# Optimization experiments

Hardware: AMD Instinct MI355X
Metric: run time of the kernel (lower is better)

Reference implementation:

```python
import jax, jax.numpy as jnp
import numpy as np

H = 16
N_JOBS = 1000000
N_MACH = 500000
NEG = -1e8

PARAM_SHAPES = [("jW1",(H,H)),("jb1",(H,)),("jW2",(H,H)),("jb2",(H,)),
                ("mW1",(H,H)),("mb1",(H,)),("mW2",(H,H)),("mb2",(H,)),
                ("aj_Wq",(H,H)),("aj_bq",(H,)),("aj_Wr",(H,H)),("aj_V",(H,)),
                ("am_Wq",(H,H)),("am_bq",(H,)),("am_Wr",(H,H)),("am_V",(H,)),
                ("ja_Wq",(H,H)),("ja_bq",(H,)),("ja_Wr",(H,H)),("ja_V",(H,)),
                ("ma_Wq",(H,H)),("ma_bq",(H,)),("ma_Wr",(H,H)),("ma_V",(H,)),
                ("g1W",(H,3*H)),("g1b",(H,)),("g2W",(H,3*H)),("g2b",(H,)),
                ("last_j",(H,))]

def setup_inputs() -> dict:
    key = jax.random.key(0)
    inp = {}
    inp["jobs"] = jax.random.normal(jax.random.fold_in(key, 0), (N_JOBS, H), dtype=jnp.float32)
    inp["machines"] = jax.random.normal(jax.random.fold_in(key, 1), (N_MACH, H), dtype=jnp.float32)
    inp["alloc_jobs_mask"] = jax.random.randint(jax.random.fold_in(key, 2), (N_JOBS,), 0, 2) > 0
    for i, (name, shape) in enumerate(PARAM_SHAPES):
        inp[name] = jax.random.normal(jax.random.fold_in(key, 10 + i), shape, dtype=jnp.float32) * 0.05
    return inp

def _emb(x, W1, b1, W2, b2):
    # custom_embedding: two tanh MLP layers (torch Linear: x @ W.T + b)
    h = jnp.tanh(x @ W1.T + b1)
    return jnp.tanh(h @ W2.T + b2)

def _att_logits(q, ref, Wq, bq, Wr, V):
    # Bahdanau additive attention: tanh(W_q q + W_r ref) @ V -> [S]
    return jnp.tanh((q @ Wq.T + bq) + ref @ Wr.T) @ V

def _query_att(q, ref, Wq, bq, Wr, V):
    # Attention with use_softmax=True followed by weighted sum over ref
    w = jax.nn.softmax(_att_logits(q, ref, Wq, bq, Wr, V))
    return w @ ref  # [H]

def reference(jobs, machines, alloc_jobs_mask,
              jW1, jb1, jW2, jb2, mW1, mb1, mW2, mb2,
              aj_Wq, aj_bq, aj_Wr, aj_V, am_Wq, am_bq, am_Wr, am_V,
              ja_Wq, ja_bq, ja_Wr, ja_V, ma_Wq, ma_bq, ma_Wr, ma_V,
              g1W, g1b, g2W, g2b, last_j):
    E_j = _emb(jobs, jW1, jb1, jW2, jb2)        # [Sj, H]
    E_m = _emb(machines, mW1, mb1, mW2, mb2)    # [Sm, H]

    # glimpse 1 conditioned on last_j
    g_j1 = _query_att(last_j, E_j, aj_Wq, aj_bq, aj_Wr, aj_V)
    g_m1 = _query_att(last_j, E_m, am_Wq, am_bq, am_Wr, am_V)
    g1 = jnp.tanh(jnp.concatenate([last_j, g_j1, g_m1]) @ g1W.T + g1b)

    # job pointer logits + invalid-action masking
    j_logits = _att_logits(g1, E_j, ja_Wq, ja_bq, ja_Wr, ja_V)
    j_logits = jnp.where(alloc_jobs_mask, j_logits, NEG)
    sel_j = jnp.argmax(j_logits)
    e_js = E_j[sel_j]

    # glimpse 2 conditioned on selected job embedding
    g_j2 = _query_att(e_js, E_j, aj_Wq, aj_bq, aj_Wr, aj_V)
    g_m2 = _query_att(e_js, E_m, am_Wq, am_bq, am_Wr, am_V)
    g2 = jnp.tanh(jnp.concatenate([e_js, g_j2, g_m2]) @ g2W.T + g2b)

    m_logits = _att_logits(g2, E_m, ma_Wq, ma_bq, ma_Wr, ma_V)
    sel_m = jnp.argmax(m_logits)

    logpas = jax.nn.log_softmax(j_logits)[sel_j] + jax.nn.log_softmax(m_logits)[sel_m]
    return sel_j, sel_m, logpas
```

## Files before the change

### kernel.cpp

```cpp
#include <hip/hip_runtime.h>
#include <cstddef>
#include <cstdint>


constexpr int NJ = 1000000;
constexpr int NM = 500000;
constexpr float NEGV = -1e8f;

constexpr int BLK = 256;
constexpr int ROWS_PER_BLK = 512;
constexpr int GB_J2 = (NJ + ROWS_PER_BLK - 1) / ROWS_PER_BLK;
constexpr int GB_M2 = (NM + ROWS_PER_BLK - 1) / ROWS_PER_BLK;
constexpr int GB_TOT2 = GB_J2 + GB_M2;

constexpr int S_QKJA = 0;
constexpr int S_QK2J = 16;
constexpr int S_QK2M = 32;
constexpr int S_EJS  = 48;
constexpr int S_QKMA = 64;
constexpr int S_LOGPJ = 80;
constexpr int S_SELJ  = 81;
constexpr int P1J = 128;
constexpr int P1M = P1J + GB_J2 * 17;
constexpr int P2V = P1M + GB_M2 * 17;
constexpr int P2I = P2V + GB_J2;
constexpr int P2L = P2I + GB_J2;

typedef float v2f __attribute__((ext_vector_type(2)));

struct Params {
    const float *jobs, *machines;
    const int *mask;
    const float *jW1, *jb1, *jW2, *jb2;
    const float *mW1, *mb1, *mW2, *mb2;
    const float *aj_Wq, *aj_bq, *aj_Wr, *aj_V;
    const float *am_Wq, *am_bq, *am_Wr, *am_V;
    const float *ja_Wq, *ja_bq, *ja_Wr, *ja_V;
    const float *ma_Wq, *ma_bq, *ma_Wr, *ma_V;
    const float *g1W, *g1b, *g2W, *g2b, *last_j;
    float *S;
    float *out;
};


__device__ __forceinline__ float fast_tanh(float x) {
    float e = __builtin_amdgcn_exp2f(x * 2.8853900817779268f);
    float r = __builtin_amdgcn_rcpf(e + 1.0f);
    return fmaf(-2.0f, r, 1.0f);
}

__device__ __forceinline__ v2f vbc(float a) { v2f r; r.x = a; r.y = a; return r; }

__device__ __forceinline__ v2f vfma(float w, v2f b, v2f c) {
    return __builtin_elementwise_fma(vbc(w), b, c);
}
__device__ __forceinline__ v2f vfma2(v2f a, v2f b, v2f c) {
    return __builtin_elementwise_fma(a, b, c);
}
__device__ __forceinline__ v2f vtanh(v2f a) {
    v2f r; r.x = fast_tanh(a.x); r.y = fast_tanh(a.y); return r;
}

__device__ __forceinline__ void load16(const float* __restrict__ X, size_t r, float (&x)[16]) {
    const float4* p4 = reinterpret_cast<const float4*>(X) + r * 4;
    float4 a = p4[0], b = p4[1], c = p4[2], d = p4[3];
    x[0]=a.x; x[1]=a.y; x[2]=a.z; x[3]=a.w;
    x[4]=b.x; x[5]=b.y; x[6]=b.z; x[7]=b.w;
    x[8]=c.x; x[9]=c.y; x[10]=c.z; x[11]=c.w;
    x[12]=d.x; x[13]=d.y; x[14]=d.z; x[15]=d.w;
}

__device__ __forceinline__ void load16_v2(const float* __restrict__ X, size_t rA, size_t rB,
                                          v2f (&x)[16]) {
    float a[16], b[16];
    load16(X, rA, a);
    load16(X, rB, b);
#pragma unroll
    for (int k = 0; k < 16; ++k) { x[k].x = a[k]; x[k].y = b[k]; }
}

__device__ __forceinline__ void emb16_v2(const v2f (&x)[16],
                                         const float* __restrict__ W1, const float* __restrict__ b1,
                                         const float* __restrict__ W2, const float* __restrict__ b2,
                                         v2f (&e)[16]) {
    v2f h[16];
#pragma unroll
    for (int i = 0; i < 16; ++i) {
        v2f a = vbc(b1[i]);
#pragma unroll
        for (int k = 0; k < 16; ++k) a = vfma(W1[i * 16 + k], x[k], a);
        h[i] = vtanh(a);
    }
#pragma unroll
    for (int i = 0; i < 16; ++i) {
        v2f a = vbc(b2[i]);
#pragma unroll
        for (int k = 0; k < 16; ++k) a = vfma(W2[i * 16 + k], h[k], a);
        e[i] = vtanh(a);
    }
}

__device__ __forceinline__ v2f att_logit_v2(const v2f (&e)[16], const float (&qk)[16],
                                            const float* __restrict__ Wr,
                                            const float* __restrict__ V) {
    v2f acc = vbc(0.0f);
#pragma unroll
    for (int i = 0; i < 16; ++i) {
        v2f r = vbc(qk[i]);
#pragma unroll
        for (int k = 0; k < 16; ++k) r = vfma(Wr[i * 16 + k], e[k], r);
        acc = vfma2(vbc(V[i]), vtanh(r), acc);
    }
    return acc;
}

__device__ __forceinline__ float wave_reduce_sum(float v) {
#pragma unroll
    for (int off = 32; off > 0; off >>= 1) v += __shfl_xor(v, off, 64);
    return v;
}

__device__ __forceinline__ void wave_reduce_argmax(float &v, int &idx) {
#pragma unroll
    for (int off = 32; off > 0; off >>= 1) {
        float ov = __shfl_xor(v, off, 64);
        int oi = __shfl_xor(idx, off, 64);
        if (ov > v || (ov == v && oi < idx)) { v = ov; idx = oi; }
    }
}

__device__ __forceinline__ float block_sum(float v) {
    __shared__ float sm[4];
    v = wave_reduce_sum(v);
    __syncthreads();
    if ((threadIdx.x & 63) == 0) sm[threadIdx.x >> 6] = v;
    __syncthreads();
    return sm[0] + sm[1] + sm[2] + sm[3];
}

__device__ __forceinline__ void block_argmax(float &v, int &i) {
    __shared__ float sv[4];
    __shared__ int si[4];
    wave_reduce_argmax(v, i);
    __syncthreads();
    if ((threadIdx.x & 63) == 0) { sv[threadIdx.x >> 6] = v; si[threadIdx.x >> 6] = i; }
    __syncthreads();
    float bv = sv[0]; int bi = si[0];
#pragma unroll
    for (int k = 1; k < 4; ++k)
        if (sv[k] > bv || (sv[k] == bv && si[k] < bi)) { bv = sv[k]; bi = si[k]; }
    v = bv; i = bi;
}

__device__ __forceinline__ void block_sum17(float l, const float (&s)[16], float* dst) {
    const int lane = threadIdx.x & 63;
    float c[8];
#pragma unroll
    for (int j = 0; j < 8; ++j) {
        const bool hi = lane & 1;
        float t = __shfl_xor(hi ? s[j] : s[j + 8], 1, 64);
        c[j] = (hi ? s[j + 8] : s[j]) + t;
    }
    float d[4];
#pragma unroll
    for (int j = 0; j < 4; ++j) {
        const bool hi = lane & 2;
        float t = __shfl_xor(hi ? c[j] : c[j + 4], 2, 64);
        d[j] = (hi ? c[j + 4] : c[j]) + t;
    }
    float e2[2];
#pragma unroll
    for (int j = 0; j < 2; ++j) {
        const bool hi = lane & 4;
        float t = __shfl_xor(hi ? d[j] : d[j + 2], 4, 64);
        e2[j] = (hi ? d[j + 2] : d[j]) + t;
    }
    float f;
    {
        const bool hi = lane & 8;
        float t = __shfl_xor(hi ? e2[0] : e2[1], 8, 64);
        f = (hi ? e2[1] : e2[0]) + t;
    }
    f += __shfl_xor(f, 16, 64);
    f += __shfl_xor(f, 32, 64);
#pragma unroll
    for (int off = 32; off > 0; off >>= 1) l += __shfl_xor(l, off, 64);

    const int idx = ((lane & 1) << 3) | ((lane & 2) << 1) | ((lane & 4) >> 1) | ((lane & 8) >> 3);
    __shared__ float red[4][17];
    const int w = threadIdx.x >> 6;
    __syncthreads();
    if (lane < 16) red[w][1 + idx] = f;
    if (lane == 0) red[w][0] = l;
    __syncthreads();
    if (threadIdx.x < 17)
        dst[threadIdx.x] = red[0][threadIdx.x] + red[1][threadIdx.x] + red[2][threadIdx.x] + red[3][threadIdx.x];
}

__global__ __launch_bounds__(BLK) void k_sweepA(Params p) {
    const bool isJob = blockIdx.x < GB_J2;
    const float* X  = isJob ? p.jobs : p.machines;
    const float* W1 = isJob ? p.jW1 : p.mW1;
    const float* b1 = isJob ? p.jb1 : p.mb1;
    const float* W2 = isJob ? p.jW2 : p.mW2;
    const float* b2 = isJob ? p.jb2 : p.mb2;
    const float* Wr = isJob ? p.aj_Wr : p.am_Wr;
    const float* V  = isJob ? p.aj_V  : p.am_V;
    const int n  = isJob ? NJ : NM;
    const int b0 = isJob ? (int)blockIdx.x : (int)blockIdx.x - GB_J2;

    __shared__ float qks[16];
    if (threadIdx.x < 16) {
        const float* Wq = isJob ? p.aj_Wq : p.am_Wq;
        const float* bq = isJob ? p.aj_bq : p.am_bq;
        const int i = threadIdx.x;
        float a = bq[i];
#pragma unroll
        for (int k = 0; k < 16; ++k) a = fmaf(Wq[i * 16 + k], p.last_j[k], a);
        qks[i] = a;
    }
    __syncthreads();
    float qk[16];
#pragma unroll
    for (int i = 0; i < 16; ++i) qk[i] = qks[i];

    const int r0 = b0 * ROWS_PER_BLK + 2 * (int)threadIdx.x;
    const bool v = r0 < n;
    const size_t a0 = (size_t)(v ? r0 : 0);
    const size_t a1 = a0 + (v ? 1 : 0);

    v2f x[16], e[16];
    load16_v2(X, a0, a1, x);
    emb16_v2(x, W1, b1, W2, b2, e);
    v2f lg = att_logit_v2(e, qk, Wr, V);
    float pw0 = v ? __expf(lg.x) : 0.0f;
    float pw1 = v ? __expf(lg.y) : 0.0f;
    float l = pw0 + pw1, s[16];
#pragma unroll
    for (int i = 0; i < 16; ++i) s[i] = fmaf(pw0, e[i].x, pw1 * e[i].y);

    block_sum17(l, s, p.S + (isJob ? P1J : P1M) + (size_t)b0 * 17);
}

__global__ __launch_bounds__(BLK) void k_combine_g(Params p, int phase) {
    const float* PJ = p.S + P1J;
    const float* PM = p.S + P1M;
    float lJ = 0.0f, lM = 0.0f, sJ[16], sM[16];
#pragma unroll
    for (int c = 0; c < 16; ++c) { sJ[c] = 0.0f; sM[c] = 0.0f; }
    for (int i = threadIdx.x; i < GB_J2; i += BLK) {
        lJ += PJ[i * 17];
#pragma unroll
        for (int c = 0; c < 16; ++c) sJ[c] += PJ[i * 17 + 1 + c];
    }
    for (int i = threadIdx.x; i < GB_M2; i += BLK) {
        lM += PM[i * 17];
#pragma unroll
        for (int c = 0; c < 16; ++c) sM[c] += PM[i * 17 + 1 + c];
    }
    __shared__ float totJ[17], totM[17];
    block_sum17(lJ, sJ, totJ);
    block_sum17(lM, sM, totM);
    __syncthreads();

    __shared__ float cb[48], gbuf[16];
    if (threadIdx.x < 16) {
        int i = threadIdx.x;
        cb[i]      = phase ? p.S[S_EJS + i] : p.last_j[i];
        cb[16 + i] = totJ[1 + i] / totJ[0];
        cb[32 + i] = totM[1 + i] / totM[0];
    }
    __syncthreads();
    const float* gW  = phase ? p.g2W : p.g1W;
    const float* gbv = phase ? p.g2b : p.g1b;
    if (threadIdx.x < 16) {
        int i = threadIdx.x;
        float a = gbv[i];
#pragma unroll
        for (int k = 0; k < 48; ++k) a = fmaf(gW[i * 48 + k], cb[k], a);
        gbuf[i] = fast_tanh(a);
    }
    __syncthreads();
    const float* Wq = phase ? p.ma_Wq : p.ja_Wq;
    const float* bq = phase ? p.ma_bq : p.ja_bq;
    const int off = phase ? S_QKMA : S_QKJA;
    if (threadIdx.x < 16) {
        int i = threadIdx.x;
        float a = bq[i];
#pragma unroll
        for (int k = 0; k < 16; ++k) a = fmaf(Wq[i * 16 + k], gbuf[k], a);
        p.S[off + i] = a;
    }
}

__global__ __launch_bounds__(BLK) void k_sweepB(Params p) {
    float qk[16];
#pragma unroll
    for (int i = 0; i < 16; ++i) qk[i] = p.S[S_QKJA + i];

    const int r0 = blockIdx.x * ROWS_PER_BLK + 2 * (int)threadIdx.x;
    const bool v = r0 < NJ;
    const size_t a0 = (size_t)(v ? r0 : 0);
    const size_t a1 = a0 + (v ? 1 : 0);

    v2f x[16], e[16];
    load16_v2(p.jobs, a0, a1, x);
    emb16_v2(x, p.jW1, p.jb1, p.jW2, p.jb2, e);
    v2f lg = att_logit_v2(e, qk, p.ja_Wr, p.ja_V);

    int2 mq = make_int2(0, 0);
    if (v) mq = *reinterpret_cast<const int2*>(p.mask + r0);
    const bool m0 = v && (mq.x != 0);
    const bool m1 = v && (mq.y != 0);
    float l = (m0 ? __expf(lg.x) : 0.0f) + (m1 ? __expf(lg.y) : 0.0f);
    float am0 = m0 ? lg.x : NEGV - 1.0f;
    float am1 = m1 ? lg.y : NEGV - 1.0f;
    float best;
    int bi;
    if (am0 >= am1) { best = am0; bi = r0; }
    else            { best = am1; bi = r0 + 1; }

    l = wave_reduce_sum(l);
    wave_reduce_argmax(best, bi);
    __shared__ float rl[4], rv[4];
    __shared__ int ri[4];
    int w = threadIdx.x >> 6, ln = threadIdx.x & 63;
    if (ln == 0) { rl[w] = l; rv[w] = best; ri[w] = bi; }
    __syncthreads();
    if (threadIdx.x == 0) {
        float L = rl[0] + rl[1] + rl[2] + rl[3];
        float vv = rv[0]; int i = ri[0];
#pragma unroll
        for (int k = 1; k < 4; ++k)
            if (rv[k] > vv || (rv[k] == vv && ri[k] < i)) { vv = rv[k]; i = ri[k]; }
        p.S[P2V + blockIdx.x] = vv;
        p.S[P2I + blockIdx.x] = (float)i;
        p.S[P2L + blockIdx.x] = L;
    }
}

__global__ __launch_bounds__(BLK) void k_combine2(Params p) {
    float v = -3.4e38f; int vi = 0x7fffffff; float l = 0.0f;
    for (int i = threadIdx.x; i < GB_J2; i += BLK) {
        float pv = p.S[P2V + i];
        int pi = (int)p.S[P2I + i];
        if (pv > v || (pv == v && pi < vi)) { v = pv; vi = pi; }
        l += p.S[P2L + i];
    }
    l = block_sum(l);
    block_argmax(v, vi);
    const int sel = vi;

    __shared__ float xb[16], hb[16], eb[16];
    if (threadIdx.x < 16) xb[threadIdx.x] = p.jobs[(size_t)sel * 16 + threadIdx.x];
    __syncthreads();
    if (threadIdx.x < 16) {
        int i = threadIdx.x;
        float a = p.jb1[i];
#pragma unroll
        for (int k = 0; k < 16; ++k) a = fmaf(p.jW1[i * 16 + k], xb[k], a);
        hb[i] = fast_tanh(a);
    }
    __syncthreads();
    if (threadIdx.x < 16) {
        int i = threadIdx.x;
        float a = p.jb2[i];
#pragma unroll
        for (int k = 0; k < 16; ++k) a = fmaf(p.jW2[i * 16 + k], hb[k], a);
        float e = fast_tanh(a);
        eb[i] = e;
        p.S[S_EJS + i] = e;
    }
    __syncthreads();
    if (threadIdx.x < 16) {
        int i = threadIdx.x;
        float a1 = p.aj_bq[i], a2 = p.am_bq[i];
#pragma unroll
        for (int k = 0; k < 16; ++k) {
            a1 = fmaf(p.aj_Wq[i * 16 + k], eb[k], a1);
            a2 = fmaf(p.am_Wq[i * 16 + k], eb[k], a2);
        }
        p.S[S_QK2J + i] = a1;
        p.S[S_QK2M + i] = a2;
    }
    if (threadIdx.x == 0) {
        p.S[S_LOGPJ] = v - logf(l);
        p.S[S_SELJ] = (float)sel;
    }
}

__global__ __launch_bounds__(BLK) void k_sweepC(Params p) {
    const bool isJob = blockIdx.x < GB_J2;
    const float* X  = isJob ? p.jobs : p.machines;
    const float* W1 = isJob ? p.jW1 : p.mW1;
    const float* b1 = isJob ? p.jb1 : p.mb1;
    const float* W2 = isJob ? p.jW2 : p.mW2;
    const float* b2 = isJob ? p.jb2 : p.mb2;
    const float* Wr = isJob ? p.aj_Wr : p.am_Wr;
    const float* V  = isJob ? p.aj_V  : p.am_V;
    const int n  = isJob ? NJ : NM;
    const int b0 = isJob ? (int)blockIdx.x : (int)blockIdx.x - GB_J2;
    const int qoff = isJob ? S_QK2J : S_QK2M;

    float qk[16];
#pragma unroll
    for (int i = 0; i < 16; ++i) qk[i] = p.S[qoff + i];

    const int r0 = b0 * ROWS_PER_BLK + 2 * (int)threadIdx.x;
    const bool v = r0 < n;
    const size_t a0 = (size_t)(v ? r0 : 0);
    const size_t a1 = a0 + (v ? 1 : 0);

    v2f x[16], e[16];
    load16_v2(X, a0, a1, x);
    emb16_v2(x, W1, b1, W2, b2, e);
    v2f lg = att_logit_v2(e, qk, Wr, V);
    float pw0 = v ? __expf(lg.x) : 0.0f;
    float pw1 = v ? __expf(lg.y) : 0.0f;
    float l = pw0 + pw1, s[16];
#pragma unroll
    for (int i = 0; i < 16; ++i) s[i] = fmaf(pw0, e[i].x, pw1 * e[i].y);

    block_sum17(l, s, p.S + (isJob ? P1J : P1M) + (size_t)b0 * 17);
}

__global__ __launch_bounds__(BLK) void k_sweepD(Params p) {
    float qk[16];
#pragma unroll
    for (int i = 0; i < 16; ++i) qk[i] = p.S[S_QKMA + i];

    const int r0 = blockIdx.x * ROWS_PER_BLK + 2 * (int)threadIdx.x;
    const bool v = r0 < NM;
    const size_t a0 = (size_t)(v ? r0 : 0);
    const size_t a1 = a0 + (v ? 1 : 0);

    v2f x[16], e[16];
    load16_v2(p.machines, a0, a1, x);
    emb16_v2(x, p.mW1, p.mb1, p.mW2, p.mb2, e);
    v2f lg = att_logit_v2(e, qk, p.ma_Wr, p.ma_V);
    float l = (v ? __expf(lg.x) : 0.0f) + (v ? __expf(lg.y) : 0.0f);
    float am0 = v ? lg.x : -3.4e38f;
    float am1 = v ? lg.y : -3.4e38f;
    float best;
    int bi;
    if (am0 >= am1) { best = am0; bi = r0; }
    else            { best = am1; bi = r0 + 1; }

    l = wave_reduce_sum(l);
    wave_reduce_argmax(best, bi);
    __shared__ float rl[4], rv[4];
    __shared__ int ri[4];
    int w = threadIdx.x >> 6, ln = threadIdx.x & 63;
    if (ln == 0) { rl[w] = l; rv[w] = best; ri[w] = bi; }
    __syncthreads();
    if (threadIdx.x == 0) {
        float L = rl[0] + rl[1] + rl[2] + rl[3];
        float vv = rv[0]; int i = ri[0];
#pragma unroll
        for (int k = 1; k < 4; ++k)
            if (rv[k] > vv || (rv[k] == vv && ri[k] < i)) { vv = rv[k]; i = ri[k]; }
        p.S[P2V + blockIdx.x] = vv;
        p.S[P2I + blockIdx.x] = (float)i;
        p.S[P2L + blockIdx.x] = L;
    }
}

__global__ __launch_bounds__(BLK) void k_combine4(Params p) {
    float v = -3.4e38f; int vi = 0x7fffffff; float l = 0.0f;
    for (int i = threadIdx.x; i < GB_M2; i += BLK) {
        float pv = p.S[P2V + i];
        int pi = (int)p.S[P2I + i];
        if (pv > v || (pv == v && pi < vi)) { v = pv; vi = pi; }
        l += p.S[P2L + i];
    }
    l = block_sum(l);
    block_argmax(v, vi);
    if (threadIdx.x == 0) {
        p.out[0] = p.S[S_SELJ];
        p.out[1] = (float)vi;
        p.out[2] = p.S[S_LOGPJ] + (v - logf(l));
    }
}

extern "C" void kernel_launch(void* const* d_in, const int* in_sizes, int n_in,
                              void* d_out, int out_size, void* d_ws, size_t ws_size,
                              hipStream_t stream) {
    Params p;
    p.jobs     = (const float*)d_in[0];
    p.machines = (const float*)d_in[1];
    p.mask     = (const int*)d_in[2];
    p.jW1 = (const float*)d_in[3];  p.jb1 = (const float*)d_in[4];
    p.jW2 = (const float*)d_in[5];  p.jb2 = (const float*)d_in[6];
    p.mW1 = (const float*)d_in[7];  p.mb1 = (const float*)d_in[8];
    p.mW2 = (const float*)d_in[9];  p.mb2 = (const float*)d_in[10];
    p.aj_Wq = (const float*)d_in[11]; p.aj_bq = (const float*)d_in[12];
    p.aj_Wr = (const float*)d_in[13]; p.aj_V  = (const float*)d_in[14];
    p.am_Wq = (const float*)d_in[15]; p.am_bq = (const float*)d_in[16];
    p.am_Wr = (const float*)d_in[17]; p.am_V  = (const float*)d_in[18];
    p.ja_Wq = (const float*)d_in[19]; p.ja_bq = (const float*)d_in[20];
    p.ja_Wr = (const float*)d_in[21]; p.ja_V  = (const float*)d_in[22];
    p.ma_Wq = (const float*)d_in[23]; p.ma_bq = (const float*)d_in[24];
    p.ma_Wr = (const float*)d_in[25]; p.ma_V  = (const float*)d_in[26];
    p.g1W = (const float*)d_in[27]; p.g1b = (const float*)d_in[28];
    p.g2W = (const float*)d_in[29]; p.g2b = (const float*)d_in[30];
    p.last_j = (const float*)d_in[31];
    p.S = (float*)d_ws;
    p.out = (float*)d_out;

    k_sweepA<<<GB_TOT2, BLK, 0, stream>>>(p);
    k_combine_g<<<1, BLK, 0, stream>>>(p, 0);
    k_sweepB<<<GB_J2, BLK, 0, stream>>>(p);
    k_combine2<<<1, BLK, 0, stream>>>(p);
    k_sweepC<<<GB_TOT2, BLK, 0, stream>>>(p);
    k_combine_g<<<1, BLK, 0, stream>>>(p, 1);
    k_sweepD<<<GB_M2, BLK, 0, stream>>>(p);
    k_combine4<<<1, BLK, 0, stream>>>(p);
}
```

Baseline: 336.0 us.

## Cache embeddings in workspace and fold combine kernels into last-block reductions

The first sweep now writes the computed job and machine embeddings to a workspace cache in a coalesced per-block layout, so the later sweeps read 16 floats per row instead of recomputing the two-layer tanh MLP. The cache is used only when the workspace is large enough. Each single-block combine kernel is replaced by a last-block-done pattern (atomic counter plus threadfence), which removes four kernel launches. A small zero kernel resets the counters and precomputes the first query projections. The trade-off is extra memory traffic for writing and re-reading about 96 MB of embeddings, plus a serial tail in the last block of each sweep.

```diff
diff --git a/kernel.cpp b/kernel.cpp
--- a/kernel.cpp
+++ b/kernel.cpp
@@ -12,6 +12,7 @@
 constexpr int GB_J2 = (NJ + ROWS_PER_BLK - 1) / ROWS_PER_BLK;
 constexpr int GB_M2 = (NM + ROWS_PER_BLK - 1) / ROWS_PER_BLK;
 constexpr int GB_TOT2 = GB_J2 + GB_M2;
+constexpr int EBLK = ROWS_PER_BLK * 16;
 
 constexpr int S_QKJA = 0;
 constexpr int S_QK2J = 16;
@@ -20,11 +21,16 @@
 constexpr int S_QKMA = 64;
 constexpr int S_LOGPJ = 80;
 constexpr int S_SELJ  = 81;
+constexpr int C_CTR   = 84;
+constexpr int S_QK1J  = 96;
+constexpr int S_QK1M  = 112;
 constexpr int P1J = 128;
 constexpr int P1M = P1J + GB_J2 * 17;
 constexpr int P2V = P1M + GB_M2 * 17;
 constexpr int P2I = P2V + GB_J2;
 constexpr int P2L = P2I + GB_J2;
+constexpr size_t E_OFF = 65536;
+static_assert(P2L + GB_J2 <= (int)E_OFF, "partials overflow into E cache");
 
 typedef float v2f __attribute__((ext_vector_type(2)));
 
@@ -39,6 +45,7 @@
     const float *ma_Wq, *ma_bq, *ma_Wr, *ma_V;
     const float *g1W, *g1b, *g2W, *g2b, *last_j;
     float *S;
+    float *Ej, *Em;
     float *out;
 };
 
@@ -79,6 +86,22 @@
     for (int k = 0; k < 16; ++k) { x[k].x = a[k]; x[k].y = b[k]; }
 }
 
+__device__ __forceinline__ void ecache_store(float* __restrict__ Eb, int t, const v2f (&e)[16]) {
+    float4* p4 = reinterpret_cast<float4*>(Eb);
+#pragma unroll
+    for (int kp = 0; kp < 8; ++kp)
+        p4[kp * 256 + t] = make_float4(e[2*kp].x, e[2*kp].y, e[2*kp+1].x, e[2*kp+1].y);
+}
+__device__ __forceinline__ void ecache_load(const float* __restrict__ Eb, int t, v2f (&e)[16]) {
+    const float4* p4 = reinterpret_cast<const float4*>(Eb);
+#pragma unroll
+    for (int kp = 0; kp < 8; ++kp) {
+        float4 q = p4[kp * 256 + t];
+        e[2*kp].x = q.x;   e[2*kp].y = q.y;
+        e[2*kp+1].x = q.z; e[2*kp+1].y = q.w;
+    }
+}
+
 __device__ __forceinline__ void emb16_v2(const v2f (&x)[16],
                                          const float* __restrict__ W1, const float* __restrict__ b1,
                                          const float* __restrict__ W2, const float* __restrict__ b2,
@@ -197,6 +220,151 @@
         dst[threadIdx.x] = red[0][threadIdx.x] + red[1][threadIdx.x] + red[2][threadIdx.x] + red[3][threadIdx.x];
 }
 
+__device__ __forceinline__ bool last_block(int* ctr, int nblocks) {
+    __shared__ int lastFlag;
+    __syncthreads();
+    __threadfence();
+    if (threadIdx.x == 0) lastFlag = (atomicAdd(ctr, 1) == nblocks - 1);
+    __syncthreads();
+    if (!lastFlag) return false;
+    __threadfence();
+    return true;
+}
+
+
+__device__ __forceinline__ void combine_g_body(const Params& p, int phase) {
+    const float* PJ = p.S + P1J;
+    const float* PM = p.S + P1M;
+    float lJ = 0.0f, lM = 0.0f, sJ[16], sM[16];
+#pragma unroll
+    for (int c = 0; c < 16; ++c) { sJ[c] = 0.0f; sM[c] = 0.0f; }
+    for (int i = threadIdx.x; i < GB_J2; i += BLK) {
+        lJ += PJ[i * 17];
+#pragma unroll
+        for (int c = 0; c < 16; ++c) sJ[c] += PJ[i * 17 + 1 + c];
+    }
+    for (int i = threadIdx.x; i < GB_M2; i += BLK) {
+        lM += PM[i * 17];
+#pragma unroll
+        for (int c = 0; c < 16; ++c) sM[c] += PM[i * 17 + 1 + c];
+    }
+    __shared__ float totJ[17], totM[17];
+    block_sum17(lJ, sJ, totJ);
+    block_sum17(lM, sM, totM);
+    __syncthreads();
+
+    __shared__ float cb[48], gbuf[16];
+    if (threadIdx.x < 16) {
+        int i = threadIdx.x;
+        cb[i]      = phase ? p.S[S_EJS + i] : p.last_j[i];
+        cb[16 + i] = totJ[1 + i] / totJ[0];
+        cb[32 + i] = totM[1 + i] / totM[0];
+    }
+    __syncthreads();
+    const float* gW  = phase ? p.g2W : p.g1W;
+    const float* gbv = phase ? p.g2b : p.g1b;
+    if (threadIdx.x < 16) {
+        int i = threadIdx.x;
+        float a = gbv[i];
+#pragma unroll
+        for (int k = 0; k < 48; ++k) a = fmaf(gW[i * 48 + k], cb[k], a);
+        gbuf[i] = fast_tanh(a);
+    }
+    __syncthreads();
+    const float* Wq = phase ? p.ma_Wq : p.ja_Wq;
+    const float* bq = phase ? p.ma_bq : p.ja_bq;
+    const int off = phase ? S_QKMA : S_QKJA;
+    if (threadIdx.x < 16) {
+        int i = threadIdx.x;
+        float a = bq[i];
+#pragma unroll
+        for (int k = 0; k < 16; ++k) a = fmaf(Wq[i * 16 + k], gbuf[k], a);
+        p.S[off + i] = a;
+    }
+}
+
+__device__ __forceinline__ void combine2_body(const Params& p) {
+    float v = -3.4e38f; int vi = 0x7fffffff; float l = 0.0f;
+    for (int i = threadIdx.x; i < GB_J2; i += BLK) {
+        float pv = p.S[P2V + i];
+        int pi = (int)p.S[P2I + i];
+        if (pv > v || (pv == v && pi < vi)) { v = pv; vi = pi; }
+        l += p.S[P2L + i];
+    }
+    l = block_sum(l);
+    block_argmax(v, vi);
+    const int sel = vi;
+
+    __shared__ float xb[16], hb[16], eb[16];
+    if (threadIdx.x < 16) xb[threadIdx.x] = p.jobs[(size_t)sel * 16 + threadIdx.x];
+    __syncthreads();
+    if (threadIdx.x < 16) {
+        int i = threadIdx.x;
+        float a = p.jb1[i];
+#pragma unroll
+        for (int k = 0; k < 16; ++k) a = fmaf(p.jW1[i * 16 + k], xb[k], a);
+        hb[i] = fast_tanh(a);
+    }
+    __syncthreads();
+    if (threadIdx.x < 16) {
+        int i = threadIdx.x;
+        float a = p.jb2[i];
+#pragma unroll
+        for (int k = 0; k < 16; ++k) a = fmaf(p.jW2[i * 16 + k], hb[k], a);
+        float e = fast_tanh(a);
+        eb[i] = e;
+        p.S[S_EJS + i] = e;
+    }
+    __syncthreads();
+    if (threadIdx.x < 16) {
+        int i = threadIdx.x;
+        float a1 = p.aj_bq[i], a2 = p.am_bq[i];
+#pragma unroll
+        for (int k = 0; k < 16; ++k) {
+            a1 = fmaf(p.aj_Wq[i * 16 + k], eb[k], a1);
+            a2 = fmaf(p.am_Wq[i * 16 + k], eb[k], a2);
+        }
+        p.S[S_QK2J + i] = a1;
+        p.S[S_QK2M + i] = a2;
+    }
+    if (threadIdx.x == 0) {
+        p.S[S_LOGPJ] = v - logf(l);
+        p.S[S_SELJ] = (float)sel;
+    }
+}
+
+__device__ __forceinline__ void combine4_body(const Params& p) {
+    float v = -3.4e38f; int vi = 0x7fffffff; float l = 0.0f;
+    for (int i = threadIdx.x; i < GB_M2; i += BLK) {
+        float pv = p.S[P2V + i];
+        int pi = (int)p.S[P2I + i];
+        if (pv > v || (pv == v && pi < vi)) { v = pv; vi = pi; }
+        l += p.S[P2L + i];
+    }
+    l = block_sum(l);
+    block_argmax(v, vi);
+    if (threadIdx.x == 0) {
+        p.out[0] = p.S[S_SELJ];
+        p.out[1] = (float)vi;
+        p.out[2] = p.S[S_LOGPJ] + (v - logf(l));
+    }
+}
+
+__global__ __launch_bounds__(64) void k_zero(Params p) {
+    if (threadIdx.x < 32) {
+        const bool isJ = threadIdx.x < 16;
+        const int i = threadIdx.x & 15;
+        const float* Wq = isJ ? p.aj_Wq : p.am_Wq;
+        const float* bq = isJ ? p.aj_bq : p.am_bq;
+        float a = bq[i];
+#pragma unroll
+        for (int k = 0; k < 16; ++k) a = fmaf(Wq[i * 16 + k], p.last_j[k], a);
+        p.S[(isJ ? S_QK1J : S_QK1M) + i] = a;
+    }
+    if (threadIdx.x >= 60) reinterpret_cast<int*>(p.S + C_CTR)[threadIdx.x - 60] = 0;
+}
+
+template <bool CACHE>
 __global__ __launch_bounds__(BLK) void k_sweepA(Params p) {
     const bool isJob = blockIdx.x < GB_J2;
     const float* X  = isJob ? p.jobs : p.machines;
@@ -206,23 +374,16 @@
     const float* b2 = isJob ? p.jb2 : p.mb2;
     const float* Wr = isJob ? p.aj_Wr : p.am_Wr;
     const float* V  = isJob ? p.aj_V  : p.am_V;
+    float* E = isJob ? p.Ej : p.Em;
     const int n  = isJob ? NJ : NM;
     const int b0 = isJob ? (int)blockIdx.x : (int)blockIdx.x - GB_J2;
 
-    __shared__ float qks[16];
-    if (threadIdx.x < 16) {
-        const float* Wq = isJob ? p.aj_Wq : p.am_Wq;
-        const float* bq = isJob ? p.aj_bq : p.am_bq;
-        const int i = threadIdx.x;
-        float a = bq[i];
-#pragma unroll
-        for (int k = 0; k < 16; ++k) a = fmaf(Wq[i * 16 + k], p.last_j[k], a);
-        qks[i] = a;
-    }
-    __syncthreads();
     float qk[16];
-#pragma unroll
-    for (int i = 0; i < 16; ++i) qk[i] = qks[i];
+    {
+        const float* src = p.S + (isJob ? S_QK1J : S_QK1M);
+#pragma unroll
+        for (int i = 0; i < 16; ++i) qk[i] = src[i];
+    }
 
     const int r0 = b0 * ROWS_PER_BLK + 2 * (int)threadIdx.x;
     const bool v = r0 < n;
@@ -232,6 +393,7 @@
     v2f x[16], e[16];
     load16_v2(X, a0, a1, x);
     emb16_v2(x, W1, b1, W2, b2, e);
+    if (CACHE) ecache_store(E + (size_t)b0 * EBLK, (int)threadIdx.x, e);
     v2f lg = att_logit_v2(e, qk, Wr, V);
     float pw0 = v ? __expf(lg.x) : 0.0f;
     float pw1 = v ? __expf(lg.y) : 0.0f;
@@ -240,59 +402,12 @@
     for (int i = 0; i < 16; ++i) s[i] = fmaf(pw0, e[i].x, pw1 * e[i].y);
 
     block_sum17(l, s, p.S + (isJob ? P1J : P1M) + (size_t)b0 * 17);
-}
-
-__global__ __launch_bounds__(BLK) void k_combine_g(Params p, int phase) {
-    const float* PJ = p.S + P1J;
-    const float* PM = p.S + P1M;
-    float lJ = 0.0f, lM = 0.0f, sJ[16], sM[16];
-#pragma unroll
-    for (int c = 0; c < 16; ++c) { sJ[c] = 0.0f; sM[c] = 0.0f; }
-    for (int i = threadIdx.x; i < GB_J2; i += BLK) {
-        lJ += PJ[i * 17];
-#pragma unroll
-        for (int c = 0; c < 16; ++c) sJ[c] += PJ[i * 17 + 1 + c];
-    }
-    for (int i = threadIdx.x; i < GB_M2; i += BLK) {
-        lM += PM[i * 17];
-#pragma unroll
-        for (int c = 0; c < 16; ++c) sM[c] += PM[i * 17 + 1 + c];
-    }
-    __shared__ float totJ[17], totM[17];
-    block_sum17(lJ, sJ, totJ);
-    block_sum17(lM, sM, totM);
-    __syncthreads();
-
-    __shared__ float cb[48], gbuf[16];
-    if (threadIdx.x < 16) {
-        int i = threadIdx.x;
-        cb[i]      = phase ? p.S[S_EJS + i] : p.last_j[i];
-        cb[16 + i] = totJ[1 + i] / totJ[0];
-        cb[32 + i] = totM[1 + i] / totM[0];
-    }
-    __syncthreads();
-    const float* gW  = phase ? p.g2W : p.g1W;
-    const float* gbv = phase ? p.g2b : p.g1b;
-    if (threadIdx.x < 16) {
-        int i = threadIdx.x;
-        float a = gbv[i];
-#pragma unroll
-        for (int k = 0; k < 48; ++k) a = fmaf(gW[i * 48 + k], cb[k], a);
-        gbuf[i] = fast_tanh(a);
-    }
-    __syncthreads();
-    const float* Wq = phase ? p.ma_Wq : p.ja_Wq;
-    const float* bq = phase ? p.ma_bq : p.ja_bq;
-    const int off = phase ? S_QKMA : S_QKJA;
-    if (threadIdx.x < 16) {
-        int i = threadIdx.x;
-        float a = bq[i];
-#pragma unroll
-        for (int k = 0; k < 16; ++k) a = fmaf(Wq[i * 16 + k], gbuf[k], a);
-        p.S[off + i] = a;
-    }
-}
-
+
+    if (last_block(reinterpret_cast<int*>(p.S + C_CTR) + 0, GB_TOT2))
+        combine_g_body(p, 0);
+}
+
+template <bool CACHE>
 __global__ __launch_bounds__(BLK) void k_sweepB(Params p) {
     float qk[16];
 #pragma unroll
@@ -303,9 +418,14 @@
     const size_t a0 = (size_t)(v ? r0 : 0);
     const size_t a1 = a0 + (v ? 1 : 0);
 
-    v2f x[16], e[16];
-    load16_v2(p.jobs, a0, a1, x);
-    emb16_v2(x, p.jW1, p.jb1, p.jW2, p.jb2, e);
+    v2f e[16];
+    if (CACHE) {
+        ecache_load(p.Ej + (size_t)blockIdx.x * EBLK, (int)threadIdx.x, e);
+    } else {
+        v2f x[16];
+        load16_v2(p.jobs, a0, a1, x);
+        emb16_v2(x, p.jW1, p.jb1, p.jW2, p.jb2, e);
+    }
     v2f lg = att_logit_v2(e, qk, p.ja_Wr, p.ja_V);
 
     int2 mq = make_int2(0, 0);
@@ -337,67 +457,22 @@
         p.S[P2I + blockIdx.x] = (float)i;
         p.S[P2L + blockIdx.x] = L;
     }
-}
-
-__global__ __launch_bounds__(BLK) void k_combine2(Params p) {
-    float v = -3.4e38f; int vi = 0x7fffffff; float l = 0.0f;
-    for (int i = threadIdx.x; i < GB_J2; i += BLK) {
-        float pv = p.S[P2V + i];
-        int pi = (int)p.S[P2I + i];
-        if (pv > v || (pv == v && pi < vi)) { v = pv; vi = pi; }
-        l += p.S[P2L + i];
-    }
-    l = block_sum(l);
-    block_argmax(v, vi);
-    const int sel = vi;
-
-    __shared__ float xb[16], hb[16], eb[16];
-    if (threadIdx.x < 16) xb[threadIdx.x] = p.jobs[(size_t)sel * 16 + threadIdx.x];
-    __syncthreads();
-    if (threadIdx.x < 16) {
-        int i = threadIdx.x;
-        float a = p.jb1[i];
-#pragma unroll
-        for (int k = 0; k < 16; ++k) a = fmaf(p.jW1[i * 16 + k], xb[k], a);
-        hb[i] = fast_tanh(a);
-    }
-    __syncthreads();
-    if (threadIdx.x < 16) {
-        int i = threadIdx.x;
-        float a = p.jb2[i];
-#pragma unroll
-        for (int k = 0; k < 16; ++k) a = fmaf(p.jW2[i * 16 + k], hb[k], a);
-        float e = fast_tanh(a);
-        eb[i] = e;
-        p.S[S_EJS + i] = e;
-    }
-    __syncthreads();
-    if (threadIdx.x < 16) {
-        int i = threadIdx.x;
-        float a1 = p.aj_bq[i], a2 = p.am_bq[i];
-#pragma unroll
-        for (int k = 0; k < 16; ++k) {
-            a1 = fmaf(p.aj_Wq[i * 16 + k], eb[k], a1);
-            a2 = fmaf(p.am_Wq[i * 16 + k], eb[k], a2);
-        }
-        p.S[S_QK2J + i] = a1;
-        p.S[S_QK2M + i] = a2;
-    }
-    if (threadIdx.x == 0) {
-        p.S[S_LOGPJ] = v - logf(l);
-        p.S[S_SELJ] = (float)sel;
-    }
-}
-
+
+    if (last_block(reinterpret_cast<int*>(p.S + C_CTR) + 1, GB_J2))
+        combine2_body(p);
+}
+
+template <bool CACHE>
 __global__ __launch_bounds__(BLK) void k_sweepC(Params p) {
     const bool isJob = blockIdx.x < GB_J2;
+    const float* Wr = isJob ? p.aj_Wr : p.am_Wr;
+    const float* V  = isJob ? p.aj_V  : p.am_V;
+    const float* E  = isJob ? p.Ej : p.Em;
     const float* X  = isJob ? p.jobs : p.machines;
     const float* W1 = isJob ? p.jW1 : p.mW1;
     const float* b1 = isJob ? p.jb1 : p.mb1;
     const float* W2 = isJob ? p.jW2 : p.mW2;
     const float* b2 = isJob ? p.jb2 : p.mb2;
-    const float* Wr = isJob ? p.aj_Wr : p.am_Wr;
-    const float* V  = isJob ? p.aj_V  : p.am_V;
     const int n  = isJob ? NJ : NM;
     const int b0 = isJob ? (int)blockIdx.x : (int)blockIdx.x - GB_J2;
     const int qoff = isJob ? S_QK2J : S_QK2M;
@@ -411,9 +486,14 @@
     const size_t a0 = (size_t)(v ? r0 : 0);
     const size_t a1 = a0 + (v ? 1 : 0);
 
-    v2f x[16], e[16];
-    load16_v2(X, a0, a1, x);
-    emb16_v2(x, W1, b1, W2, b2, e);
+    v2f e[16];
+    if (CACHE) {
+        ecache_load(E + (size_t)b0 * EBLK, (int)threadIdx.x, e);
+    } else {
+        v2f x[16];
+        load16_v2(X, a0, a1, x);
+        emb16_v2(x, W1, b1, W2, b2, e);
+    }
     v2f lg = att_logit_v2(e, qk, Wr, V);
     float pw0 = v ? __expf(lg.x) : 0.0f;
     float pw1 = v ? __expf(lg.y) : 0.0f;
@@ -422,8 +502,12 @@
     for (int i = 0; i < 16; ++i) s[i] = fmaf(pw0, e[i].x, pw1 * e[i].y);
 
     block_sum17(l, s, p.S + (isJob ? P1J : P1M) + (size_t)b0 * 17);
-}
-
+
+    if (last_block(reinterpret_cast<int*>(p.S + C_CTR) + 2, GB_TOT2))
+        combine_g_body(p, 1);
+}
+
+template <bool CACHE>
 __global__ __launch_bounds__(BLK) void k_sweepD(Params p) {
     float qk[16];
 #pragma unroll
@@ -434,9 +518,14 @@
     const size_t a0 = (size_t)(v ? r0 : 0);
     const size_t a1 = a0 + (v ? 1 : 0);
 
-    v2f x[16], e[16];
-    load16_v2(p.machines, a0, a1, x);
-    emb16_v2(x, p.mW1, p.mb1, p.mW2, p.mb2, e);
+    v2f e[16];
+    if (CACHE) {
+        ecache_load(p.Em + (size_t)blockIdx.x * EBLK, (int)threadIdx.x, e);
+    } else {
+        v2f x[16];
+        load16_v2(p.machines, a0, a1, x);
+        emb16_v2(x, p.mW1, p.mb1, p.mW2, p.mb2, e);
+    }
     v2f lg = att_logit_v2(e, qk, p.ma_Wr, p.ma_V);
     float l = (v ? __expf(lg.x) : 0.0f) + (v ? __expf(lg.y) : 0.0f);
     float am0 = v ? lg.x : -3.4e38f;
@@ -463,23 +552,9 @@
         p.S[P2I + blockIdx.x] = (float)i;
         p.S[P2L + blockIdx.x] = L;
     }
-}
-
-__global__ __launch_bounds__(BLK) void k_combine4(Params p) {
-    float v = -3.4e38f; int vi = 0x7fffffff; float l = 0.0f;
-    for (int i = threadIdx.x; i < GB_M2; i += BLK) {
-        float pv = p.S[P2V + i];
-        int pi = (int)p.S[P2I + i];
-        if (pv > v || (pv == v && pi < vi)) { v = pv; vi = pi; }
-        l += p.S[P2L + i];
-    }
-    l = block_sum(l);
-    block_argmax(v, vi);
-    if (threadIdx.x == 0) {
-        p.out[0] = p.S[S_SELJ];
-        p.out[1] = (float)vi;
-        p.out[2] = p.S[S_LOGPJ] + (v - logf(l));
-    }
+
+    if (last_block(reinterpret_cast<int*>(p.S + C_CTR) + 3, GB_M2))
+        combine4_body(p);
 }
 
 extern "C" void kernel_launch(void* const* d_in, const int* in_sizes, int n_in,
@@ -505,14 +580,23 @@
     p.g2W = (const float*)d_in[29]; p.g2b = (const float*)d_in[30];
     p.last_j = (const float*)d_in[31];
     p.S = (float*)d_ws;
+    p.Ej = (float*)d_ws + E_OFF;
+    p.Em = p.Ej + (size_t)GB_J2 * EBLK;
     p.out = (float*)d_out;
 
-    k_sweepA<<<GB_TOT2, BLK, 0, stream>>>(p);
-    k_combine_g<<<1, BLK, 0, stream>>>(p, 0);
-    k_sweepB<<<GB_J2, BLK, 0, stream>>>(p);
-    k_combine2<<<1, BLK, 0, stream>>>(p);
-    k_sweepC<<<GB_TOT2, BLK, 0, stream>>>(p);
-    k_combine_g<<<1, BLK, 0, stream>>>(p, 1);
-    k_sweepD<<<GB_M2, BLK, 0, stream>>>(p);
-    k_combine4<<<1, BLK, 0, stream>>>(p);
-}
+    const size_t needed = (E_OFF + (size_t)GB_TOT2 * EBLK) * sizeof(float);
+    const bool cache = ws_size >= needed;
+
+    k_zero<<<1, 64, 0, stream>>>(p);
+    if (cache) {
+        k_sweepA<true><<<GB_TOT2, BLK, 0, stream>>>(p);
+        k_sweepB<true><<<GB_J2, BLK, 0, stream>>>(p);
+        k_sweepC<true><<<GB_TOT2, BLK, 0, stream>>>(p);
+        k_sweepD<true><<<GB_M2, BLK, 0, stream>>>(p);
+    } else {
+        k_sweepA<false><<<GB_TOT2, BLK, 0, stream>>>(p);
+        k_sweepB<false><<<GB_J2, BLK, 0, stream>>>(p);
+        k_sweepC<false><<<GB_TOT2, BLK, 0, stream>>>(p);
+        k_sweepD<false><<<GB_M2, BLK, 0, stream>>>(p);
+    }
+}
```

New measurement: 1.022 ms. 204% more time.

## Cache job and machine embeddings in workspace and reuse them across sweeps

Applied to the files above, without the earlier changes.

The first sweep now writes the computed job and machine embeddings to a workspace buffer in a coalesced float4 layout. The three later sweeps load those embeddings instead of re-reading the raw inputs and re-running the two-layer tanh MLP. This removes repeated embedding arithmetic, which dominates these sweeps. The cost is an extra write of all embeddings in the first pass and a dependence on a large workspace; without enough space the code falls back to recomputing.

```diff
diff --git a/kernel.cpp b/kernel.cpp
--- a/kernel.cpp
+++ b/kernel.cpp
@@ -12,6 +12,7 @@
 constexpr int GB_J2 = (NJ + ROWS_PER_BLK - 1) / ROWS_PER_BLK;
 constexpr int GB_M2 = (NM + ROWS_PER_BLK - 1) / ROWS_PER_BLK;
 constexpr int GB_TOT2 = GB_J2 + GB_M2;
+constexpr int EBLK = ROWS_PER_BLK * 16;
 
 constexpr int S_QKJA = 0;
 constexpr int S_QK2J = 16;
@@ -25,6 +26,8 @@
 constexpr int P2V = P1M + GB_M2 * 17;
 constexpr int P2I = P2V + GB_J2;
 constexpr int P2L = P2I + GB_J2;
+constexpr size_t E_OFF = 65536;
+static_assert(P2L + GB_J2 <= (int)E_OFF, "partials overflow into E cache");
 
 typedef float v2f __attribute__((ext_vector_type(2)));
 
@@ -39,6 +42,7 @@
     const float *ma_Wq, *ma_bq, *ma_Wr, *ma_V;
     const float *g1W, *g1b, *g2W, *g2b, *last_j;
     float *S;
+    float *Ej, *Em;
     float *out;
 };
 
@@ -79,6 +83,22 @@
     for (int k = 0; k < 16; ++k) { x[k].x = a[k]; x[k].y = b[k]; }
 }
 
+__device__ __forceinline__ void ecache_store(float* __restrict__ Eb, int t, const v2f (&e)[16]) {
+    float4* p4 = reinterpret_cast<float4*>(Eb);
+#pragma unroll
+    for (int kp = 0; kp < 8; ++kp)
+        p4[kp * 256 + t] = make_float4(e[2*kp].x, e[2*kp].y, e[2*kp+1].x, e[2*kp+1].y);
+}
+__device__ __forceinline__ void ecache_load(const float* __restrict__ Eb, int t, v2f (&e)[16]) {
+    const float4* p4 = reinterpret_cast<const float4*>(Eb);
+#pragma unroll
+    for (int kp = 0; kp < 8; ++kp) {
+        float4 q = p4[kp * 256 + t];
+        e[2*kp].x = q.x;   e[2*kp].y = q.y;
+        e[2*kp+1].x = q.z; e[2*kp+1].y = q.w;
+    }
+}
+
 __device__ __forceinline__ void emb16_v2(const v2f (&x)[16],
                                          const float* __restrict__ W1, const float* __restrict__ b1,
                                          const float* __restrict__ W2, const float* __restrict__ b2,
@@ -197,7 +217,8 @@
         dst[threadIdx.x] = red[0][threadIdx.x] + red[1][threadIdx.x] + red[2][threadIdx.x] + red[3][threadIdx.x];
 }
 
-__global__ __launch_bounds__(BLK) void k_sweepA(Params p) {
+template <bool CACHE>
+__global__ __launch_bounds__(BLK) void k_emb_g1(Params p) {
     const bool isJob = blockIdx.x < GB_J2;
     const float* X  = isJob ? p.jobs : p.machines;
     const float* W1 = isJob ? p.jW1 : p.mW1;
@@ -206,6 +227,7 @@
     const float* b2 = isJob ? p.jb2 : p.mb2;
     const float* Wr = isJob ? p.aj_Wr : p.am_Wr;
     const float* V  = isJob ? p.aj_V  : p.am_V;
+    float* E = isJob ? p.Ej : p.Em;
     const int n  = isJob ? NJ : NM;
     const int b0 = isJob ? (int)blockIdx.x : (int)blockIdx.x - GB_J2;
 
@@ -232,6 +254,7 @@
     v2f x[16], e[16];
     load16_v2(X, a0, a1, x);
     emb16_v2(x, W1, b1, W2, b2, e);
+    if (CACHE) ecache_store(E + (size_t)b0 * EBLK, (int)threadIdx.x, e);
     v2f lg = att_logit_v2(e, qk, Wr, V);
     float pw0 = v ? __expf(lg.x) : 0.0f;
     float pw1 = v ? __expf(lg.y) : 0.0f;
@@ -293,7 +316,8 @@
     }
 }
 
-__global__ __launch_bounds__(BLK) void k_sweepB(Params p) {
+template <bool CACHE>
+__global__ __launch_bounds__(BLK) void k_jlogits(Params p) {
     float qk[16];
 #pragma unroll
     for (int i = 0; i < 16; ++i) qk[i] = p.S[S_QKJA + i];
@@ -303,9 +327,14 @@
     const size_t a0 = (size_t)(v ? r0 : 0);
     const size_t a1 = a0 + (v ? 1 : 0);
 
-    v2f x[16], e[16];
-    load16_v2(p.jobs, a0, a1, x);
-    emb16_v2(x, p.jW1, p.jb1, p.jW2, p.jb2, e);
+    v2f e[16];
+    if (CACHE) {
+        ecache_load(p.Ej + (size_t)blockIdx.x * EBLK, (int)threadIdx.x, e);
+    } else {
+        v2f x[16];
+        load16_v2(p.jobs, a0, a1, x);
+        emb16_v2(x, p.jW1, p.jb1, p.jW2, p.jb2, e);
+    }
     v2f lg = att_logit_v2(e, qk, p.ja_Wr, p.ja_V);
 
     int2 mq = make_int2(0, 0);
@@ -389,15 +418,17 @@
     }
 }
 
-__global__ __launch_bounds__(BLK) void k_sweepC(Params p) {
+template <bool CACHE>
+__global__ __launch_bounds__(BLK) void k_glimpse2(Params p) {
     const bool isJob = blockIdx.x < GB_J2;
+    const float* Wr = isJob ? p.aj_Wr : p.am_Wr;
+    const float* V  = isJob ? p.aj_V  : p.am_V;
+    const float* E  = isJob ? p.Ej : p.Em;
     const float* X  = isJob ? p.jobs : p.machines;
     const float* W1 = isJob ? p.jW1 : p.mW1;
     const float* b1 = isJob ? p.jb1 : p.mb1;
     const float* W2 = isJob ? p.jW2 : p.mW2;
     const float* b2 = isJob ? p.jb2 : p.mb2;
-    const float* Wr = isJob ? p.aj_Wr : p.am_Wr;
-    const float* V  = isJob ? p.aj_V  : p.am_V;
     const int n  = isJob ? NJ : NM;
     const int b0 = isJob ? (int)blockIdx.x : (int)blockIdx.x - GB_J2;
     const int qoff = isJob ? S_QK2J : S_QK2M;
@@ -411,9 +442,14 @@
     const size_t a0 = (size_t)(v ? r0 : 0);
     const size_t a1 = a0 + (v ? 1 : 0);
 
-    v2f x[16], e[16];
-    load16_v2(X, a0, a1, x);
-    emb16_v2(x, W1, b1, W2, b2, e);
+    v2f e[16];
+    if (CACHE) {
+        ecache_load(E + (size_t)b0 * EBLK, (int)threadIdx.x, e);
+    } else {
+        v2f x[16];
+        load16_v2(X, a0, a1, x);
+        emb16_v2(x, W1, b1, W2, b2, e);
+    }
     v2f lg = att_logit_v2(e, qk, Wr, V);
     float pw0 = v ? __expf(lg.x) : 0.0f;
     float pw1 = v ? __expf(lg.y) : 0.0f;
@@ -424,7 +460,8 @@
     block_sum17(l, s, p.S + (isJob ? P1J : P1M) + (size_t)b0 * 17);
 }
 
-__global__ __launch_bounds__(BLK) void k_sweepD(Params p) {
+template <bool CACHE>
+__global__ __launch_bounds__(BLK) void k_mlogits(Params p) {
     float qk[16];
 #pragma unroll
     for (int i = 0; i < 16; ++i) qk[i] = p.S[S_QKMA + i];
@@ -434,9 +471,14 @@
     const size_t a0 = (size_t)(v ? r0 : 0);
     const size_t a1 = a0 + (v ? 1 : 0);
 
-    v2f x[16], e[16];
-    load16_v2(p.machines, a0, a1, x);
-    emb16_v2(x, p.mW1, p.mb1, p.mW2, p.mb2, e);
+    v2f e[16];
+    if (CACHE) {
+        ecache_load(p.Em + (size_t)blockIdx.x * EBLK, (int)threadIdx.x, e);
+    } else {
+        v2f x[16];
+        load16_v2(p.machines, a0, a1, x);
+        emb16_v2(x, p.mW1, p.mb1, p.mW2, p.mb2, e);
+    }
     v2f lg = att_logit_v2(e, qk, p.ma_Wr, p.ma_V);
     float l = (v ? __expf(lg.x) : 0.0f) + (v ? __expf(lg.y) : 0.0f);
     float am0 = v ? lg.x : -3.4e38f;
@@ -505,14 +547,30 @@
     p.g2W = (const float*)d_in[29]; p.g2b = (const float*)d_in[30];
     p.last_j = (const float*)d_in[31];
     p.S = (float*)d_ws;
+    p.Ej = (float*)d_ws + E_OFF;
+    p.Em = p.Ej + (size_t)GB_J2 * EBLK;
     p.out = (float*)d_out;
 
-    k_sweepA<<<GB_TOT2, BLK, 0, stream>>>(p);
-    k_combine_g<<<1, BLK, 0, stream>>>(p, 0);
-    k_sweepB<<<GB_J2, BLK, 0, stream>>>(p);
-    k_combine2<<<1, BLK, 0, stream>>>(p);
-    k_sweepC<<<GB_TOT2, BLK, 0, stream>>>(p);
-    k_combine_g<<<1, BLK, 0, stream>>>(p, 1);
-    k_sweepD<<<GB_M2, BLK, 0, stream>>>(p);
-    k_combine4<<<1, BLK, 0, stream>>>(p);
-}
+    const size_t needed = (E_OFF + (size_t)GB_TOT2 * EBLK) * sizeof(float);
+    const bool cache = ws_size >= needed;
+
+    if (cache) {
+        k_emb_g1<true><<<GB_TOT2, BLK, 0, stream>>>(p);
+        k_combine_g<<<1, BLK, 0, stream>>>(p, 0);
+        k_jlogits<true><<<GB_J2, BLK, 0, stream>>>(p);
+        k_combine2<<<1, BLK, 0, stream>>>(p);
+        k_glimpse2<true><<<GB_TOT2, BLK, 0, stream>>>(p);
+        k_combine_g<<<1, BLK, 0, stream>>>(p, 1);
+        k_mlogits<true><<<GB_M2, BLK, 0, stream>>>(p);
+        k_combine4<<<1, BLK, 0, stream>>>(p);
+    } else {
+        k_emb_g1<false><<<GB_TOT2, BLK, 0, stream>>>(p);
+        k_combine_g<<<1, BLK, 0, stream>>>(p, 0);
+        k_jlogits<false><<<GB_J2, BLK, 0, stream>>>(p);
+        k_combine2<<<1, BLK, 0, stream>>>(p);
+        k_glimpse2<false><<<GB_TOT2, BLK, 0, stream>>>(p);
+        k_combine_g<<<1, BLK, 0, stream>>>(p, 1);
+        k_mlogits<false><<<GB_M2, BLK, 0, stream>>>(p);
+        k_combine4<<<1, BLK, 0, stream>>>(p);
+    }
+}
```

Result: faster. 292.6 us (-12.9%).
